# Performance work log

Hardware: AMD Instinct MI355X
Metric: run time of the kernel (lower is better)

## Reference

```python
import jax, jax.numpy as jnp
import numpy as np

B, S, E, H = 2, 2048, 1024, 16
D = E // H  # head_dim
SCALE = 1.0 / np.sqrt(D)


def rope_tables(seq_len, dim, dtype=jnp.float32):
    # matches RotaryEmbedding: inv_freq over even indices, emb = cat([freqs, freqs])
    inv_freq = 1.0 / (10000.0 ** (jnp.arange(0, dim, 2, dtype=dtype) / dim))
    t = jnp.arange(seq_len, dtype=dtype)
    freqs = t[:, None] * inv_freq[None, :]          # [S, D/2]
    emb = jnp.concatenate([freqs, freqs], axis=-1)  # [S, D]
    return jnp.cos(emb)[None, None], jnp.sin(emb)[None, None]  # [1,1,S,D]


def apply_rope(x, cos, sin):
    # x: [B,H,S,D]; interleaved rotate exactly as the torch code:
    # x2 = stack([-x[...,1::2], x[...,0::2]], -1).reshape_as(x)
    x2 = jnp.stack([-x[..., 1::2], x[..., 0::2]], axis=-1).reshape(x.shape)
    return x * cos + x2 * sin


def setup_inputs() -> dict:
    key = jax.random.key(0)
    ks = jax.random.split(key, 12)
    std = 1.0 / np.sqrt(E)
    inp = {
        "query": jax.random.normal(ks[0], (B, S, E), jnp.float32),
        "key": jax.random.normal(ks[1], (B, S, E), jnp.float32),
        "value": jax.random.normal(ks[2], (B, S, E), jnp.float32),
        "mask": jnp.ones((B, S), jnp.int32),
        "Wq": jax.random.normal(ks[3], (E, E), jnp.float32) * std,
        "bq": jax.random.normal(ks[4], (E,), jnp.float32) * std,
        "Wk": jax.random.normal(ks[5], (E, E), jnp.float32) * std,
        "bk": jax.random.normal(ks[6], (E,), jnp.float32) * std,
        "Wv": jax.random.normal(ks[7], (E, E), jnp.float32) * std,
        "bv": jax.random.normal(ks[8], (E,), jnp.float32) * std,
        "Wo": jax.random.normal(ks[9], (E, E), jnp.float32) * std,
        "bo": jax.random.normal(ks[10], (E,), jnp.float32) * std,
    }
    return inp


def reference(query, key, value, mask, Wq, bq, Wk, bk, Wv, bv, Wo, bo):
    b, sq, _ = query.shape
    sk = key.shape[1]
    # linear projections (torch Linear: x @ W.T + b), split into heads [B,H,S,D]
    Q = (query @ Wq.T + bq).reshape(b, sq, H, D).transpose(0, 2, 1, 3)
    K = (key @ Wk.T + bk).reshape(b, sk, H, D).transpose(0, 2, 1, 3)
    V = (value @ Wv.T + bv).reshape(b, sk, H, D).transpose(0, 2, 1, 3)
    cos_q, sin_q = rope_tables(sq, D)
    cos_k, sin_k = rope_tables(sk, D)
    Q = apply_rope(Q, cos_q, sin_q)
    K = apply_rope(K, cos_k, sin_k)
    scores = jnp.einsum("bhqd,bhkd->bhqk", Q, K) * SCALE
    neg_inf = jnp.finfo(scores.dtype).min
    scores = jnp.where(mask[:, None, None, :] == 0, neg_inf, scores)
    attn = jax.nn.softmax(scores, axis=-1)
    # dropout omitted (deterministic reference / eval mode)
    out = jnp.einsum("bhqk,bhkd->bhqd", attn, V)
    out = out.transpose(0, 2, 1, 3).reshape(b, sq, E)
    return out @ Wo.T + bo
```

## Files before the change

### kernel.cpp

```cpp
#include <hip/hip_runtime.h>
#include <stdint.h>

typedef unsigned short u16;
typedef __bf16 bf16x8 __attribute__((ext_vector_type(8)));
typedef float f32x4 __attribute__((ext_vector_type(4)));
typedef float f32x2 __attribute__((ext_vector_type(2)));
typedef u16 u16x4v __attribute__((ext_vector_type(4)));

#define DI __device__ __forceinline__

constexpr int BB = 2, SS = 2048, EE = 1024, HH = 16, DD = 64;
constexpr int MROWS = BB * SS;
constexpr int KDIM = 1024, NDIM = 1024;

DI u16 f2bf(float f) {
  uint32_t u = __float_as_uint(f);
  return (u16)((u + 0x7FFFu + ((u >> 16) & 1u)) >> 16);
}
DI float bf2f(u16 h) { return __uint_as_float(((uint32_t)h) << 16); }

DI uint32_t cvtpk_bf16(float a, float b) {
  uint32_t r;
  asm("v_cvt_pk_bf16_f32 %0, %1, %2" : "=v"(r) : "v"(a), "v"(b));
  return r;
}

DI void cp16(const void* g, void* lds) {
  __builtin_amdgcn_global_load_lds((const __attribute__((address_space(1))) void*)g,
                                   (__attribute__((address_space(3))) void*)lds, 16, 0, 0);
}

DI f32x4 mfma16(bf16x8 a, bf16x8 b, f32x4 c) {
  return __builtin_amdgcn_mfma_f32_16x16x32_bf16(a, b, c, 0, 0, 0);
}

__global__ __launch_bounds__(256) void prep_cast(
    const float* __restrict__ q, const float* __restrict__ k, const float* __restrict__ v,
    const float* __restrict__ wq, const float* __restrict__ wk, const float* __restrict__ wv,
    const float* __restrict__ wo,
    u16* __restrict__ qb, u16* __restrict__ kb, u16* __restrict__ vb,
    u16* __restrict__ wqb, u16* __restrict__ wkb, u16* __restrict__ wvb,
    u16* __restrict__ wob) {
  constexpr size_t SZI = (size_t)MROWS * EE;
  constexpr size_t SZW = (size_t)EE * EE;
  const size_t g = ((size_t)blockIdx.x * 256 + threadIdx.x) * 4;
  const float* src; u16* dst; size_t o;
  if (g < SZI)          { src = q; dst = qb; o = g; }
  else if (g < 2 * SZI) { src = k; dst = kb; o = g - SZI; }
  else if (g < 3 * SZI) { src = v; dst = vb; o = g - 2 * SZI; }
  else {
    size_t t2 = g - 3 * SZI;
    int wi = (int)(t2 / SZW);
    o = t2 - (size_t)(wi < 4 ? wi : 3) * SZW;
    src = wi == 0 ? wq : wi == 1 ? wk : wi == 2 ? wv : wo;
    dst = wi == 0 ? wqb : wi == 1 ? wkb : wi == 2 ? wvb : wob;
  }
  const float4 f = *(const float4*)(src + o);
  u16x4v hv;
  hv[0] = f2bf(f.x); hv[1] = f2bf(f.y); hv[2] = f2bf(f.z); hv[3] = f2bf(f.w);
  *(u16x4v*)(dst + o) = hv;
}

__global__ __launch_bounds__(256) void rope_tables_k(float* __restrict__ csT) {
  const int t = blockIdx.x * 256 + threadIdx.x;
  const int s = t >> 6, d = t & 63, j = d & 31;
  const float ang = (float)s * exp2f(-(float)j * 0.4152410118f);
  float2 cs; cs.x = cosf(ang); cs.y = sinf(ang);
  ((float2*)csT)[t] = cs;
}

__global__ __launch_bounds__(256) void gemm_qkv(
    const u16* __restrict__ qb, const u16* __restrict__ kb, const u16* __restrict__ vb,
    const u16* __restrict__ wqb, const u16* __restrict__ wkb, const u16* __restrict__ wvb,
    const float* __restrict__ bq, const float* __restrict__ bk, const float* __restrict__ bv,
    u16* __restrict__ Qp, u16* __restrict__ Kp, u16* __restrict__ Vtg,
    const float* __restrict__ csT) {
  __shared__ alignas(16) u16 sA[128 * 64];
  __shared__ alignas(16) u16 sB[128 * 64];
  const int tsel = blockIdx.y >> 5;
  const bool vtr = (tsel == 2);
  const u16* A    = tsel == 0 ? wqb : tsel == 1 ? wkb : vb;
  const u16* Bm   = tsel == 0 ? qb  : tsel == 1 ? kb  : wvb;
  const float* bias = tsel == 0 ? bq : tsel == 1 ? bk : bv;

  const int fBase = blockIdx.x * 128;
  const int tBase = (blockIdx.y & 31) * 128;
  const int aBase = vtr ? tBase : fBase;
  const int bBase = vtr ? fBase : tBase;
  const int tid = threadIdx.x;
  const int lane = tid & 63, w = tid >> 6;
  const int quad = lane >> 4, l16 = lane & 15;
  const int wr = w >> 1, wc = w & 1;

  size_t aSrc[4], bSrc[4];
  u16 *aDst[4], *bDst[4];
#pragma unroll
  for (int j = 0; j < 4; ++j) {
    const int c = tid + j * 256;
    const int row = c >> 3, sl = c & 7;
    const size_t off = (size_t)row * KDIM + ((sl ^ (row & 7)) * 8);
    aSrc[j] = (size_t)aBase * KDIM + off; aDst[j] = &sA[c * 8];
    bSrc[j] = (size_t)bBase * KDIM + off; bDst[j] = &sB[c * 8];
  }

  f32x4 acc[4][4];
#pragma unroll
  for (int mi = 0; mi < 4; ++mi)
#pragma unroll
    for (int ni = 0; ni < 4; ++ni)
#pragma unroll
      for (int e = 0; e < 4; ++e) acc[mi][ni][e] = 0.f;

  const int arow = wr * 64 + l16, brow = wc * 64 + l16;

  for (int k0 = 0; k0 < KDIM; k0 += 64) {
    __syncthreads();
#pragma unroll
    for (int j = 0; j < 4; ++j) {
      cp16(A + aSrc[j] + k0, aDst[j]);
      cp16(Bm + bSrc[j] + k0, bDst[j]);
    }
    __syncthreads();
#pragma unroll
    for (int h = 0; h < 2; ++h) {
      bf16x8 af[4], bf[4];
#pragma unroll
      for (int i = 0; i < 4; ++i) {
        const int ar = arow + i * 16, br = brow + i * 16;
        af[i] = *(const bf16x8*)&sA[ar * 64 + (((h * 4 + quad) ^ (ar & 7)) << 3)];
        bf[i] = *(const bf16x8*)&sB[br * 64 + (((h * 4 + quad) ^ (br & 7)) << 3)];
      }
#pragma unroll
      for (int mi = 0; mi < 4; ++mi)
#pragma unroll
        for (int ni = 0; ni < 4; ++ni)
          acc[mi][ni] = mfma16(af[mi], bf[ni], acc[mi][ni]);
    }
  }

  if (!vtr) {
    u16* C = tsel == 0 ? Qp : Kp;
#pragma unroll
    for (int mi = 0; mi < 4; ++mi) {
      const int fm = fBase + wr * 64 + mi * 16 + quad * 4;
      const float4 b4 = *(const float4*)&bias[fm];
      const int d0 = fm & 63;
#pragma unroll
      for (int ni = 0; ni < 4; ++ni) {
        const int t = tBase + wc * 64 + ni * 16 + l16;
        const int srow = t & (SS - 1);
        const float* cs = &csT[(size_t)((srow << 6) + d0) * 2];
        const float4 cs01 = *(const float4*)cs;
        const float4 cs23 = *(const float4*)(cs + 4);
        const float v0 = acc[mi][ni][0] + b4.x;
        const float v1 = acc[mi][ni][1] + b4.y;
        const float v2 = acc[mi][ni][2] + b4.z;
        const float v3 = acc[mi][ni][3] + b4.w;
        const float o0 = v0 * cs01.x - v1 * cs01.y;
        const float o1 = v1 * cs01.z + v0 * cs01.w;
        const float o2 = v2 * cs23.x - v3 * cs23.y;
        const float o3 = v3 * cs23.z + v2 * cs23.w;
        uint2 pk;
        pk.x = cvtpk_bf16(o0, o1);
        pk.y = cvtpk_bf16(o2, o3);
        *(uint2*)&C[(size_t)t * NDIM + fm] = pk;
      }
    }
  } else {
#pragma unroll
    for (int ni = 0; ni < 4; ++ni) {
      const int f = fBase + wc * 64 + ni * 16 + l16;
      const int h = f >> 6, d = f & 63;
      const float bb = bias[f];
#pragma unroll
      for (int mi = 0; mi < 4; ++mi) {
        const int t0 = tBase + wr * 64 + mi * 16 + quad * 4;
        const int b = t0 >> 11, s0 = t0 & (SS - 1);
        const int sp0 = (s0 & ~31) | (((s0 >> 2) & 3) << 3) | (((s0 >> 4) & 1) << 2);
        uint2 pk;
        pk.x = cvtpk_bf16(acc[mi][ni][0] + bb, acc[mi][ni][1] + bb);
        pk.y = cvtpk_bf16(acc[mi][ni][2] + bb, acc[mi][ni][3] + bb);
        *(uint2*)&Vtg[((size_t)((b * 16 + h) * 64 + d)) * SS + sp0] = pk;
      }
    }
  }
}

__global__ __launch_bounds__(512, 4) void attn_kernel(
    const u16* __restrict__ Qp, const u16* __restrict__ Kp, const u16* __restrict__ Vtg,
    const int* __restrict__ mask, u16* __restrict__ Oh) {
  __shared__ alignas(16) u16 sK[128 * 64];
  __shared__ alignas(16) u16 sVt[64 * 128];
  __shared__ float sMask[128];
  const int tid = threadIdx.x, lane = tid & 63, w = tid >> 6;
  const int quad = lane >> 4, l16 = lane & 15;
  const int bh = blockIdx.y, b = bh >> 4, h = bh & 15;
  const int q0 = blockIdx.x * 128 + w * 16;
  const u16* Qb = Qp + (size_t)b * SS * EE + h * DD;
  const u16* Kb = Kp + (size_t)b * SS * EE + h * DD;
  const u16* Vb = Vtg + (size_t)bh * DD * SS;
  constexpr float C1 = 0.18033688011112042f;
  constexpr float FM = 12.0f;
  constexpr float MNEG = -30000.f;

  bf16x8 qf[2];
#pragma unroll
  for (int ks = 0; ks < 2; ++ks)
    qf[ks] = *(const bf16x8*)(Qb + (size_t)(q0 + l16) * EE + ks * 32 + quad * 8);

  f32x4 oacc[4];
#pragma unroll
  for (int nd = 0; nd < 4; ++nd)
#pragma unroll
    for (int e = 0; e < 4; ++e) oacc[nd][e] = 0.f;
  f32x2 sum2 = {0.f, 0.f};

  for (int kt = 0; kt < SS / 128; ++kt) {
    const int key0 = kt * 128;
    __syncthreads();
#pragma unroll
    for (int i = 0; i < 2; ++i) {
      const int c = i * 512 + tid;
      const int key = c >> 3;
      const int g8 = ((c & 7) ^ (key & 7)) * 8;
      cp16(Kb + (size_t)(key0 + key) * EE + g8, &sK[c * 8]);
    }
#pragma unroll
    for (int i = 0; i < 2; ++i) {
      const int L = i * 512 + tid;
      const int d = L >> 4;
      const int g8 = ((L & 15) ^ (d & 15)) * 8;
      cp16(Vb + (size_t)d * SS + key0 + g8, &sVt[L * 8]);
    }
    if (tid < 128) sMask[tid] = mask[b * SS + key0 + tid] ? -FM : MNEG;
    __syncthreads();

    f32x4 sacc[8];
#pragma unroll
    for (int ni = 0; ni < 8; ++ni)
#pragma unroll
      for (int e = 0; e < 4; ++e) sacc[ni][e] = 0.f;
#pragma unroll
    for (int ks = 0; ks < 2; ++ks)
#pragma unroll
      for (int ni = 0; ni < 8; ++ni) {
        const int row = ni * 16 + l16;
        const bf16x8 kf = *(const bf16x8*)&sK[row * 64 + (((ks * 4 + quad) ^ (l16 & 7)) << 3)];
        sacc[ni] = mfma16(kf, qf[ks], sacc[ni]);
      }

    uint32_t pw32[4][4];
#pragma unroll
    for (int ni = 0; ni < 8; ++ni) {
      const int kb4 = ni * 16 + quad * 4;
      const f32x2 m01 = *(const f32x2*)&sMask[kb4];
      const f32x2 m23 = *(const f32x2*)&sMask[kb4 + 2];
      f32x2 t01, t23;
      t01.x = sacc[ni][0]; t01.y = sacc[ni][1];
      t23.x = sacc[ni][2]; t23.y = sacc[ni][3];
      t01 = t01 * C1 + m01;
      t23 = t23 * C1 + m23;
      f32x2 p01, p23;
      p01.x = exp2f(t01.x); p01.y = exp2f(t01.y);
      p23.x = exp2f(t23.x); p23.y = exp2f(t23.y);
      sum2 += p01;
      sum2 += p23;
      const int k2 = ni >> 1, j2 = (ni & 1) * 2;
      pw32[k2][j2]     = cvtpk_bf16(p01.x, p01.y);
      pw32[k2][j2 + 1] = cvtpk_bf16(p23.x, p23.y);
    }

#pragma unroll
    for (int k2 = 0; k2 < 4; ++k2) {
      union { uint32_t u[4]; bf16x8 v; } pf;
#pragma unroll
      for (int j = 0; j < 4; ++j) pf.u[j] = pw32[k2][j];
#pragma unroll
      for (int nd = 0; nd < 4; ++nd) {
        const int row = nd * 16 + l16;
        const bf16x8 vf = *(const bf16x8*)&sVt[row * 128 + (((k2 * 4 + quad) ^ l16) << 3)];
        oacc[nd] = mfma16(pf.v, vf, oacc[nd]);
      }
    }
  }

  float lrow = sum2.x + sum2.y;
  lrow += __shfl_xor(lrow, 16, 64);
  lrow += __shfl_xor(lrow, 32, 64);
  const float linv = lrow > 0.f ? 1.0f / lrow : 0.f;

#pragma unroll
  for (int r = 0; r < 4; ++r) {
    const float li = __shfl(linv, quad * 4 + r, 16);
    const size_t row = (size_t)(b * SS + q0 + quad * 4 + r) * EE + h * DD;
#pragma unroll
    for (int nd = 0; nd < 4; ++nd) {
      const int d = nd * 16 + l16;
      Oh[row + d] = f2bf(oacc[nd][r] * li);
    }
  }
}

__global__ __launch_bounds__(256) void gemm_out(
    const u16* __restrict__ Ab, const u16* __restrict__ Bb,
    const float* __restrict__ bias, float* __restrict__ Cout) {
  __shared__ alignas(16) u16 sA[128 * 64];
  __shared__ alignas(16) u16 sB[64 * 64];
  const int rowBase = blockIdx.y * 128;
  const int colBase = blockIdx.x * 64;
  const int tid = threadIdx.x;
  const int lane = tid & 63, w = tid >> 6;
  const int quad = lane >> 4, l16 = lane & 15;
  const int wr = w >> 1, wc = w & 1;

  size_t aSrc[4]; u16* aDst[4];
  size_t bSrc[2]; u16* bDst[2];
#pragma unroll
  for (int j = 0; j < 4; ++j) {
    const int c = tid + j * 256;
    const int row = c >> 3, sl = c & 7;
    aSrc[j] = (size_t)(rowBase + row) * KDIM + ((sl ^ (row & 7)) * 8);
    aDst[j] = &sA[c * 8];
  }
#pragma unroll
  for (int j = 0; j < 2; ++j) {
    const int c = tid + j * 256;
    const int row = c >> 3, sl = c & 7;
    bSrc[j] = (size_t)(colBase + row) * KDIM + ((sl ^ (row & 7)) * 8);
    bDst[j] = &sB[c * 8];
  }

  f32x4 acc[4][2];
#pragma unroll
  for (int mi = 0; mi < 4; ++mi)
#pragma unroll
    for (int ni = 0; ni < 2; ++ni)
#pragma unroll
      for (int e = 0; e < 4; ++e) acc[mi][ni][e] = 0.f;

  const int arow = wr * 64 + l16, brow = wc * 32 + l16;

  for (int k0 = 0; k0 < KDIM; k0 += 64) {
    __syncthreads();
#pragma unroll
    for (int j = 0; j < 4; ++j) cp16(Ab + aSrc[j] + k0, aDst[j]);
#pragma unroll
    for (int j = 0; j < 2; ++j) cp16(Bb + bSrc[j] + k0, bDst[j]);
    __syncthreads();
#pragma unroll
    for (int h = 0; h < 2; ++h) {
      bf16x8 af[4], bf[2];
#pragma unroll
      for (int i = 0; i < 4; ++i) {
        const int ar = arow + i * 16;
        af[i] = *(const bf16x8*)&sA[ar * 64 + (((h * 4 + quad) ^ (ar & 7)) << 3)];
      }
#pragma unroll
      for (int i = 0; i < 2; ++i) {
        const int br = brow + i * 16;
        bf[i] = *(const bf16x8*)&sB[br * 64 + (((h * 4 + quad) ^ (br & 7)) << 3)];
      }
#pragma unroll
      for (int mi = 0; mi < 4; ++mi)
#pragma unroll
        for (int ni = 0; ni < 2; ++ni)
          acc[mi][ni] = mfma16(af[mi], bf[ni], acc[mi][ni]);
    }
  }

#pragma unroll
  for (int mi = 0; mi < 4; ++mi) {
    const int rb = rowBase + wr * 64 + mi * 16 + quad * 4;
#pragma unroll
    for (int ni = 0; ni < 2; ++ni) {
      const int col = colBase + wc * 32 + ni * 16 + l16;
      const float bb = bias[col];
#pragma unroll
      for (int r = 0; r < 4; ++r)
        Cout[(size_t)(rb + r) * NDIM + col] = acc[mi][ni][r] + bb;
    }
  }
}

extern "C" void kernel_launch(void* const* d_in, const int* in_sizes, int n_in,
                              void* d_out, int out_size, void* d_ws, size_t ws_size,
                              hipStream_t stream) {
  const float* q    = (const float*)d_in[0];
  const float* k    = (const float*)d_in[1];
  const float* v    = (const float*)d_in[2];
  const int*   mask = (const int*)d_in[3];
  const float* Wq = (const float*)d_in[4];
  const float* bq = (const float*)d_in[5];
  const float* Wk = (const float*)d_in[6];
  const float* bk = (const float*)d_in[7];
  const float* Wv = (const float*)d_in[8];
  const float* bv = (const float*)d_in[9];
  const float* Wo = (const float*)d_in[10];
  const float* bo = (const float*)d_in[11];
  float* out = (float*)d_out;
  char* ws = (char*)d_ws;
  constexpr size_t MB = 1024 * 1024;
  u16* qb  = (u16*)(ws + 0 * MB);
  u16* kb  = (u16*)(ws + 8 * MB);
  u16* vb  = (u16*)(ws + 16 * MB);
  u16* wqb = (u16*)(ws + 24 * MB);
  u16* wkb = (u16*)(ws + 26 * MB);
  u16* wvb = (u16*)(ws + 28 * MB);
  u16* wob = (u16*)(ws + 30 * MB);
  u16* Qp  = (u16*)(ws + 32 * MB);
  u16* Kp  = (u16*)(ws + 40 * MB);
  u16* Vtg = (u16*)(ws + 48 * MB);
  u16* oh  = (u16*)(ws + 56 * MB);
  float* csT = (float*)(ws + 64 * MB);

  prep_cast<<<16384, 256, 0, stream>>>(q, k, v, Wq, Wk, Wv, Wo,
                                       qb, kb, vb, wqb, wkb, wvb, wob);
  rope_tables_k<<<512, 256, 0, stream>>>(csT);
  gemm_qkv<<<dim3(8, 96), 256, 0, stream>>>(qb, kb, vb, wqb, wkb, wvb,
                                            bq, bk, bv, Qp, Kp, Vtg, csT);
  attn_kernel<<<dim3(16, 32), 512, 0, stream>>>(Qp, Kp, Vtg, mask, oh);
  gemm_out<<<dim3(16, 32), 256, 0, stream>>>(oh, wob, bo, out);
}
```

Before: 250.4 us.

## Split attention keys into two halves and add combine kernel; fuse rope tables into cast

The attention kernel now splits the key range into two halves, each handled by a separate block, which doubles the grid to 1024 blocks and raises the occupancy hint. Each half writes an unnormalized partial output and a row sum. A new combine kernel adds the two partials and normalizes them. This relies on the fixed max offset used in the softmax, so partials can simply be summed. The rope table kernel is folded into the cast kernel to save one launch. The cost is extra global traffic for the partial outputs plus one more kernel launch.

```diff
diff --git a/kernel.cpp b/kernel.cpp
--- a/kernel.cpp
+++ b/kernel.cpp
@@ -40,9 +40,17 @@
     const float* __restrict__ wo,
     u16* __restrict__ qb, u16* __restrict__ kb, u16* __restrict__ vb,
     u16* __restrict__ wqb, u16* __restrict__ wkb, u16* __restrict__ wvb,
-    u16* __restrict__ wob) {
+    u16* __restrict__ wob, float* __restrict__ csT) {
   constexpr size_t SZI = (size_t)MROWS * EE;
   constexpr size_t SZW = (size_t)EE * EE;
+  if (blockIdx.x >= 16384) {
+    const int t = (blockIdx.x - 16384) * 256 + threadIdx.x;
+    const int s = t >> 6, d = t & 63, j = d & 31;
+    const float ang = (float)s * exp2f(-(float)j * 0.4152410118f);
+    float2 cs; cs.x = cosf(ang); cs.y = sinf(ang);
+    ((float2*)csT)[t] = cs;
+    return;
+  }
   const size_t g = ((size_t)blockIdx.x * 256 + threadIdx.x) * 4;
   const float* src; u16* dst; size_t o;
   if (g < SZI)          { src = q; dst = qb; o = g; }
@@ -51,7 +59,7 @@
   else {
     size_t t2 = g - 3 * SZI;
     int wi = (int)(t2 / SZW);
-    o = t2 - (size_t)(wi < 4 ? wi : 3) * SZW;
+    o = t2 - (size_t)wi * SZW;
     src = wi == 0 ? wq : wi == 1 ? wk : wi == 2 ? wv : wo;
     dst = wi == 0 ? wqb : wi == 1 ? wkb : wi == 2 ? wvb : wob;
   }
@@ -59,14 +67,6 @@
   u16x4v hv;
   hv[0] = f2bf(f.x); hv[1] = f2bf(f.y); hv[2] = f2bf(f.z); hv[3] = f2bf(f.w);
   *(u16x4v*)(dst + o) = hv;
-}
-
-__global__ __launch_bounds__(256) void rope_tables_k(float* __restrict__ csT) {
-  const int t = blockIdx.x * 256 + threadIdx.x;
-  const int s = t >> 6, d = t & 63, j = d & 31;
-  const float ang = (float)s * exp2f(-(float)j * 0.4152410118f);
-  float2 cs; cs.x = cosf(ang); cs.y = sinf(ang);
-  ((float2*)csT)[t] = cs;
 }
 
 __global__ __launch_bounds__(256) void gemm_qkv(
@@ -186,16 +186,17 @@
   }
 }
 
-__global__ __launch_bounds__(512, 4) void attn_kernel(
+__global__ __launch_bounds__(512, 8) void attn_kernel(
     const u16* __restrict__ Qp, const u16* __restrict__ Kp, const u16* __restrict__ Vtg,
-    const int* __restrict__ mask, u16* __restrict__ Oh) {
+    const int* __restrict__ mask, u16* __restrict__ Op, float* __restrict__ lp) {
   __shared__ alignas(16) u16 sK[128 * 64];
   __shared__ alignas(16) u16 sVt[64 * 128];
   __shared__ float sMask[128];
   const int tid = threadIdx.x, lane = tid & 63, w = tid >> 6;
   const int quad = lane >> 4, l16 = lane & 15;
-  const int bh = blockIdx.y, b = bh >> 4, h = bh & 15;
-  const int q0 = blockIdx.x * 128 + w * 16;
+  const int bh = blockIdx.x, b = bh >> 4, h = bh & 15;
+  const int khalf = blockIdx.y & 1, qt = blockIdx.y >> 1;
+  const int q0 = qt * 128 + w * 16;
   const u16* Qb = Qp + (size_t)b * SS * EE + h * DD;
   const u16* Kb = Kp + (size_t)b * SS * EE + h * DD;
   const u16* Vb = Vtg + (size_t)bh * DD * SS;
@@ -215,7 +216,7 @@
     for (int e = 0; e < 4; ++e) oacc[nd][e] = 0.f;
   f32x2 sum2 = {0.f, 0.f};
 
-  for (int kt = 0; kt < SS / 128; ++kt) {
+  for (int kt = khalf * 8; kt < khalf * 8 + 8; ++kt) {
     const int key0 = kt * 128;
     __syncthreads();
 #pragma unroll
@@ -287,18 +288,45 @@
   float lrow = sum2.x + sum2.y;
   lrow += __shfl_xor(lrow, 16, 64);
   lrow += __shfl_xor(lrow, 32, 64);
-  const float linv = lrow > 0.f ? 1.0f / lrow : 0.f;
-
+  if (lane < 16)
+    lp[(size_t)khalf * (BB * HH * SS) + (size_t)bh * SS + q0 + lane] = lrow;
+
+  u16* Od = Op + (size_t)khalf * MROWS * EE;
 #pragma unroll
   for (int r = 0; r < 4; ++r) {
-    const float li = __shfl(linv, quad * 4 + r, 16);
     const size_t row = (size_t)(b * SS + q0 + quad * 4 + r) * EE + h * DD;
 #pragma unroll
     for (int nd = 0; nd < 4; ++nd) {
       const int d = nd * 16 + l16;
-      Oh[row + d] = f2bf(oacc[nd][r] * li);
-    }
-  }
+      Od[row + d] = f2bf(oacc[nd][r]);
+    }
+  }
+}
+
+__global__ __launch_bounds__(256) void attn_combine(
+    const u16* __restrict__ Op, const float* __restrict__ lp, u16* __restrict__ oh) {
+  const int t = blockIdx.x * 256 + threadIdx.x;
+  const int token = t >> 7, col0 = (t & 127) * 8;
+  const int b = token >> 11, q = token & (SS - 1), h = col0 >> 6;
+  const int bh = b * 16 + h;
+  const float l0 = lp[(size_t)bh * SS + q];
+  const float l1 = lp[(size_t)(BB * HH * SS) + (size_t)bh * SS + q];
+  const float inv = 1.0f / (l0 + l1);
+  const size_t off = (size_t)token * EE + col0;
+  const uint4 a = *(const uint4*)&Op[off];
+  const uint4 c = *(const uint4*)&Op[(size_t)MROWS * EE + off];
+  uint4 r;
+  const uint32_t au[4] = {a.x, a.y, a.z, a.w};
+  const uint32_t cu[4] = {c.x, c.y, c.z, c.w};
+  uint32_t ru[4];
+#pragma unroll
+  for (int i = 0; i < 4; ++i) {
+    const float lo = (__uint_as_float(au[i] << 16) + __uint_as_float(cu[i] << 16)) * inv;
+    const float hi = (__uint_as_float(au[i] & 0xFFFF0000u) + __uint_as_float(cu[i] & 0xFFFF0000u)) * inv;
+    ru[i] = cvtpk_bf16(lo, hi);
+  }
+  r.x = ru[0]; r.y = ru[1]; r.z = ru[2]; r.w = ru[3];
+  *(uint4*)&oh[off] = r;
 }
 
 __global__ __launch_bounds__(256) void gemm_out(
@@ -412,12 +440,14 @@
   u16* Vtg = (u16*)(ws + 48 * MB);
   u16* oh  = (u16*)(ws + 56 * MB);
   float* csT = (float*)(ws + 64 * MB);
-
-  prep_cast<<<16384, 256, 0, stream>>>(q, k, v, Wq, Wk, Wv, Wo,
-                                       qb, kb, vb, wqb, wkb, wvb, wob);
-  rope_tables_k<<<512, 256, 0, stream>>>(csT);
+  u16* Op  = (u16*)(ws + 66 * MB);
+  float* lp = (float*)(ws + 82 * MB);
+
+  prep_cast<<<16896, 256, 0, stream>>>(q, k, v, Wq, Wk, Wv, Wo,
+                                       qb, kb, vb, wqb, wkb, wvb, wob, csT);
   gemm_qkv<<<dim3(8, 96), 256, 0, stream>>>(qb, kb, vb, wqb, wkb, wvb,
                                             bq, bk, bv, Qp, Kp, Vtg, csT);
-  attn_kernel<<<dim3(16, 32), 512, 0, stream>>>(Qp, Kp, Vtg, mask, oh);
+  attn_kernel<<<dim3(32, 32), 512, 0, stream>>>(Qp, Kp, Vtg, mask, Op, lp);
+  attn_combine<<<2048, 256, 0, stream>>>(Op, lp, oh);
   gemm_out<<<dim3(16, 32), 256, 0, stream>>>(oh, wob, bo, out);
 }
```

Measured after the change: 355.7 us. +42.1%, slower.
